# Kernel optimization log

Hardware: AMD Instinct MI355X
Metric: run time of the kernel (lower is better)

## Reference

```python
import jax, jax.numpy as jnp
import numpy as np

DIM = 768
NUM_HEADS = 16
HEAD_DIM = DIM // NUM_HEADS        # 48
AXIS_DIM = HEAD_DIM // 3           # 16 dims per spatial axis (t, y, x)
ROPE_BASE = 10000.0
T, H, W = 8, 14, 14                # N = 1568


def setup_inputs() -> dict:
    key = jax.random.key(0)
    k1, k2, k3 = jax.random.split(key, 3)
    B, N = 4, T * H * W
    x = jax.random.normal(k1, (B, N, DIM), dtype=jnp.float32)
    # 3D position grid (t, y, x) for each token
    t, y, xg = np.meshgrid(np.arange(T), np.arange(H), np.arange(W), indexing="ij")
    pos = jnp.asarray(np.stack([t.ravel(), y.ravel(), xg.ravel()], axis=-1), dtype=jnp.int32)  # [N,3]
    W_qkv = jax.random.normal(k2, (DIM, 3 * DIM), dtype=jnp.float32) * (DIM ** -0.5)
    W_proj = jax.random.normal(k3, (DIM, DIM), dtype=jnp.float32) * (DIM ** -0.5)
    b_proj = jnp.zeros((DIM,), dtype=jnp.float32)
    return {"x": x, "pos": pos, "W_qkv": W_qkv, "W_proj": W_proj, "b_proj": b_proj}


def _rope3d(q, k, pos):
    # q, k: [B, H, N, HEAD_DIM]; pos: [N, 3] int
    half = AXIS_DIM // 2  # 8 frequency pairs per axis
    inv_freq = ROPE_BASE ** (-jnp.arange(half, dtype=jnp.float32) / half)  # [half]
    # angles per axis: [N, 3, half]
    ang = pos.astype(jnp.float32)[:, :, None] * inv_freq[None, None, :]
    cos = jnp.cos(ang)  # [N, 3, half]
    sin = jnp.sin(ang)

    def rotate(t):
        # split head_dim into 3 axis chunks of AXIS_DIM, rotate_half within each
        t3 = t.reshape(*t.shape[:-1], 3, AXIS_DIM)          # [B,H,N,3,AXIS_DIM]
        t1, t2 = t3[..., :half], t3[..., half:]             # [B,H,N,3,half]
        c = cos[None, None]                                  # [1,1,N,3,half]
        s = sin[None, None]
        r = jnp.concatenate([t1 * c - t2 * s, t2 * c + t1 * s], axis=-1)
        return r.reshape(*t.shape)

    return rotate(q), rotate(k)


def reference(x, pos, W_qkv, W_proj, b_proj):
    B, N, C = x.shape
    scale = 1.0 / jnp.sqrt(jnp.asarray(HEAD_DIM, dtype=x.dtype))
    qkv = (x @ W_qkv).reshape(B, N, 3, NUM_HEADS, HEAD_DIM)
    qkv = jnp.transpose(qkv, (2, 0, 3, 1, 4))               # [3,B,H,N,Dh]
    q, k, v = qkv[0], qkv[1], qkv[2]
    q, k = _rope3d(q, k, pos)
    attn = jnp.einsum("bhnd,bhmd->bhnm", q, k) * scale      # [B,H,N,N]
    attn = jax.nn.softmax(attn, axis=-1)
    out = jnp.einsum("bhnm,bhmd->bhnd", attn, v)            # [B,H,N,Dh]
    out = jnp.transpose(out, (0, 2, 1, 3)).reshape(B, N, C)
    return out @ W_proj + b_proj
```

## Files before the change

kernel.cpp:

```cpp
#include <hip/hip_runtime.h>
#include <hip/hip_bf16.h>
#include <math.h>

#define DIM 768
#define NHEADS 16
#define HD 48
#define NTOK 1568
#define BATCH 4
#define ROWS (BATCH * NTOK)
#define QKV_COLS (3 * DIM)

typedef __attribute__((ext_vector_type(8))) _Float16 f16x8;
typedef __attribute__((ext_vector_type(2))) __fp16 fp16v2;
typedef __attribute__((ext_vector_type(4))) float f32x4;

__device__ inline ushort f2h(float f) {
    union { _Float16 h; ushort u; } v; v.h = (_Float16)f; return v.u;
}
__device__ inline float h2f(ushort u) {
    union { _Float16 h; ushort u; } v; v.u = u; return (float)v.h;
}

__device__ inline void gl16(const void* g, void* l) {
    __builtin_amdgcn_global_load_lds(
        (const __attribute__((address_space(1))) unsigned int*)g,
        (__attribute__((address_space(3))) unsigned int*)l, 16, 0, 0);
}

__global__ void cast_f32_f16(const float* __restrict__ in, ushort* __restrict__ out, int n4) {
    int i = blockIdx.x * blockDim.x + threadIdx.x;
    if (i >= n4) return;
    float4 v = ((const float4*)in)[i];
    ushort4 o;
    o.x = f2h(v.x); o.y = f2h(v.y); o.z = f2h(v.z); o.w = f2h(v.w);
    ((ushort4*)out)[i] = o;
}

__global__ void transpose_cast(const float* __restrict__ in, ushort* __restrict__ out,
                               int R, int C) {
    __shared__ ushort tile[32][33];
    int tx = threadIdx.x, ty = threadIdx.y;
    int c0 = blockIdx.x * 32, r0 = blockIdx.y * 32;
#pragma unroll
    for (int k = 0; k < 4; ++k)
        tile[ty + 8 * k][tx] = f2h(in[(size_t)(r0 + ty + 8 * k) * C + c0 + tx]);
    __syncthreads();
#pragma unroll
    for (int k = 0; k < 4; ++k)
        out[(size_t)(c0 + ty + 8 * k) * R + r0 + tx] = tile[tx][ty + 8 * k];
}

#define GBK 64

template <int BM>
__global__ __launch_bounds__(256) void gemm_f16(
    const ushort* __restrict__ A, const ushort* __restrict__ Bt,
    float* __restrict__ Cf, ushort* __restrict__ Cb, ushort* __restrict__ Vt,
    const float* __restrict__ bias, int M, int N, int K) {
    constexpr int MI = BM / 32;
    __shared__ ushort sA[2][BM * 64];
    __shared__ ushort sB[2][128 * 64];
    const int tid = threadIdx.x;
    const int wid = tid >> 6, lane = tid & 63;
    const int wm = wid >> 1, wn = wid & 1;
    const int m0 = blockIdx.y * BM, n0 = blockIdx.x * 128;
    const int lr = lane & 15, g = lane >> 4;

    auto STAGE = [&](int buf, int k0) {
#pragma unroll
        for (int i = 0; i < MI; ++i) {
            int c = tid + 256 * i;
            int row = c >> 3;
            int ch = (c & 7) ^ (row & 7);
            gl16(&A[(size_t)(m0 + row) * K + k0 + ch * 8], &sA[buf][(c & ~63) * 8]);
        }
#pragma unroll
        for (int i = 0; i < 4; ++i) {
            int c = tid + 256 * i;
            int row = c >> 3;
            int ch = (c & 7) ^ (row & 7);
            gl16(&Bt[(size_t)(n0 + row) * K + k0 + ch * 8], &sB[buf][(c & ~63) * 8]);
        }
    };

    f32x4 acc[MI][4] = {};
    const int NK = K / GBK;
    STAGE(0, 0);
    for (int t = 0; t < NK; ++t) {
        const int cur = t & 1;
        asm volatile("s_waitcnt vmcnt(0)" ::: "memory");
        __builtin_amdgcn_s_barrier();
        if (t + 1 < NK) STAGE(cur ^ 1, (t + 1) * GBK);
#pragma unroll
        for (int k2 = 0; k2 < GBK; k2 += 32) {
            f16x8 af[MI], bg[4];
#pragma unroll
            for (int f = 0; f < MI; ++f) {
                int ra = wm * (BM / 2) + f * 16 + lr;
                int ba = (ra * 128 + k2 * 2 + g * 16) ^ ((ra & 7) << 4);
                af[f] = *(const f16x8*)((const char*)sA[cur] + ba);
            }
#pragma unroll
            for (int f = 0; f < 4; ++f) {
                int rb = wn * 64 + f * 16 + lr;
                int bb = (rb * 128 + k2 * 2 + g * 16) ^ ((rb & 7) << 4);
                bg[f] = *(const f16x8*)((const char*)sB[cur] + bb);
            }
#pragma unroll
            for (int mi = 0; mi < MI; ++mi)
#pragma unroll
                for (int ni = 0; ni < 4; ++ni)
                    acc[mi][ni] = __builtin_amdgcn_mfma_f32_16x16x32_f16(
                        bg[ni], af[mi], acc[mi][ni], 0, 0, 0);
        }
    }
    const bool vpath = (Vt != nullptr) && (n0 >= 2 * DIM);
#pragma unroll
    for (int mi = 0; mi < MI; ++mi) {
        int m = m0 + wm * (BM / 2) + mi * 16 + lr;
#pragma unroll
        for (int ni = 0; ni < 4; ++ni) {
            int nb = n0 + wn * 64 + ni * 16 + g * 4;
            if (Cf) {
                float4 b4 = *(const float4*)&bias[nb];
                float4 o4;
                o4.x = acc[mi][ni][0] + b4.x;
                o4.y = acc[mi][ni][1] + b4.y;
                o4.z = acc[mi][ni][2] + b4.z;
                o4.w = acc[mi][ni][3] + b4.w;
                *(float4*)&Cf[(size_t)m * N + nb] = o4;
            } else if (vpath) {
                int bb = m / NTOK, tok = m % NTOK;
#pragma unroll
                for (int j = 0; j < 4; ++j)
                    Vt[((size_t)bb * DIM + (nb - 2 * DIM + j)) * NTOK + tok] =
                        f2h(acc[mi][ni][j]);
            } else {
                union { fp16v2 h; uint u; } c0, c1;
                c0.h = __builtin_amdgcn_cvt_pkrtz(acc[mi][ni][0], acc[mi][ni][1]);
                c1.h = __builtin_amdgcn_cvt_pkrtz(acc[mi][ni][2], acc[mi][ni][3]);
                uint2 uu; uu.x = c0.u; uu.y = c1.u;
                *(uint2*)&Cb[(size_t)m * N + nb] = uu;
            }
        }
    }
}

__global__ void rope_f16(ushort* __restrict__ qkv, const int* __restrict__ pos) {
    int idx = blockIdx.x * blockDim.x + threadIdx.x;
    const int total = BATCH * NTOK * NHEADS * 3;
    if (idx >= total) return;
    int axis = idx % 3; int t = idx / 3;
    int h = t & 15; t >>= 4;
    int n = t % NTOK; int b = t / NTOK;

    float p = (float)pos[n * 3 + axis];
    size_t base = ((size_t)b * NTOK + n) * QKV_COLS + h * HD + axis * 16;

    ushort lo[8], hi[8], klo[8], khi[8];
    *(ushort4*)&lo[0] = *(ushort4*)&qkv[base];
    *(ushort4*)&lo[4] = *(ushort4*)&qkv[base + 4];
    *(ushort4*)&hi[0] = *(ushort4*)&qkv[base + 8];
    *(ushort4*)&hi[4] = *(ushort4*)&qkv[base + 12];
    *(ushort4*)&klo[0] = *(ushort4*)&qkv[base + DIM];
    *(ushort4*)&klo[4] = *(ushort4*)&qkv[base + DIM + 4];
    *(ushort4*)&khi[0] = *(ushort4*)&qkv[base + DIM + 8];
    *(ushort4*)&khi[4] = *(ushort4*)&qkv[base + DIM + 12];

    const float RINV = 0.31622776601683794f;
    float fj = 1.0f;
#pragma unroll
    for (int j = 0; j < 8; ++j) {
        float s, c; __sincosf(p * fj, &s, &c); fj *= RINV;
        float q1 = h2f(lo[j]), q2 = h2f(hi[j]);
        lo[j] = f2h(q1 * c - q2 * s);
        hi[j] = f2h(q2 * c + q1 * s);
        float k1 = h2f(klo[j]), k2 = h2f(khi[j]);
        klo[j] = f2h(k1 * c - k2 * s);
        khi[j] = f2h(k2 * c + k1 * s);
    }
    *(ushort4*)&qkv[base] = *(ushort4*)&lo[0];
    *(ushort4*)&qkv[base + 4] = *(ushort4*)&lo[4];
    *(ushort4*)&qkv[base + 8] = *(ushort4*)&hi[0];
    *(ushort4*)&qkv[base + 12] = *(ushort4*)&hi[4];
    *(ushort4*)&qkv[base + DIM] = *(ushort4*)&klo[0];
    *(ushort4*)&qkv[base + DIM + 4] = *(ushort4*)&klo[4];
    *(ushort4*)&qkv[base + DIM + 8] = *(ushort4*)&khi[0];
    *(ushort4*)&qkv[base + DIM + 12] = *(ushort4*)&khi[4];
}

#define QBLK 128
#define KVB 32
#define NT (NTOK / KVB)
#define PP 40

__global__ __launch_bounds__(256) void attn_mfma(const ushort* __restrict__ qkv,
                                                 const ushort* __restrict__ vt,
                                                 ushort* __restrict__ aout) {
    __shared__ ushort sK3[3][KVB * 64];
    __shared__ ushort sV3[3][64 * 32];
    __shared__ ushort sP[4][32 * PP];
    const int tid = threadIdx.x, w = tid >> 6, lane = tid & 63;
    const int b = blockIdx.x >> 4, h = blockIdx.x & 15;
    const int q0 = blockIdx.y * QBLK;
    const size_t bbase = (size_t)b * NTOK * QKV_COLS;
    const size_t vbase = ((size_t)b * DIM + h * HD) * NTOK;
    const int lr = lane & 15, g = lane >> 4, lk = g << 3;
    const float qs = 0.14433756729740643f * 1.4426950408889634f;
    const float M2 = 14.0f;

    if (tid < 32) {
        sV3[0][48 * 32 + tid] = 0x3C00;
        sV3[1][48 * 32 + tid] = 0x3C00;
        sV3[2][48 * 32 + tid] = 0x3C00;
    }
    asm volatile("s_waitcnt lgkmcnt(0)" ::: "memory");

    f16x8 aq[2][2];
#pragma unroll
    for (int rb = 0; rb < 2; ++rb) {
        int qr = q0 + w * 32 + rb * 16 + lr;
        if (qr >= NTOK) qr = NTOK - 1;
        const ushort* qp = &qkv[bbase + (size_t)qr * QKV_COLS + h * HD];
        ushort r0[8], r1[8];
        *(ushort4*)&r0[0] = *(const ushort4*)&qp[lk];
        *(ushort4*)&r0[4] = *(const ushort4*)&qp[lk + 4];
        if (g < 2) {
            *(ushort4*)&r1[0] = *(const ushort4*)&qp[32 + lk];
            *(ushort4*)&r1[4] = *(const ushort4*)&qp[32 + lk + 4];
        } else {
#pragma unroll
            for (int e = 0; e < 8; ++e) r1[e] = 0;
        }
        f16x8 a0, a1;
#pragma unroll
        for (int e = 0; e < 8; ++e) {
            a0[e] = (_Float16)(h2f(r0[e]) * qs);
            a1[e] = (_Float16)(h2f(r1[e]) * qs);
        }
        aq[rb][0] = a0; aq[rb][1] = a1;
    }

    auto STAGE = [&](int buf, int kv0) {
        {
            int c = tid, row = c >> 3;
            int ch = (c & 7) ^ (row & 7);
            gl16(&qkv[bbase + (size_t)(kv0 + row) * QKV_COLS + DIM + h * HD + ch * 8],
                 &sK3[buf][(c & ~63) * 8]);
        }
        if (lane < 48) {
            int c = w * 48 + lane, d = c >> 2;
            int cc = (c & 3) ^ ((d >> 1) & 3);
            gl16(&vt[vbase + (size_t)d * NTOK + kv0 + cc * 8],
                 &sV3[buf][w * 384]);
        }
    };

    f32x4 o[2][4] = {};

    STAGE(0, 0);
    STAGE(1, KVB);
    for (int t = 0; t < NT; ++t) {
        const int cur = t % 3;
        if (t + 1 < NT) asm volatile("s_waitcnt vmcnt(2)" ::: "memory");
        else            asm volatile("s_waitcnt vmcnt(0)" ::: "memory");
        __builtin_amdgcn_s_barrier();
        if (t + 2 < NT) STAGE((t + 2) % 3, (t + 2) * KVB);

        f16x8 bk[2][2];
#pragma unroll
        for (int f = 0; f < 2; ++f)
#pragma unroll
            for (int ks = 0; ks < 2; ++ks) {
                int row = f * 16 + lr;
                int byt = (row * 128 + ks * 64 + g * 16) ^ ((lr & 7) << 4);
                bk[f][ks] = *(const f16x8*)((const char*)sK3[cur] + byt);
            }
        f32x4 sacc[2][2] = {{{-M2, -M2, -M2, -M2}, {-M2, -M2, -M2, -M2}},
                            {{-M2, -M2, -M2, -M2}, {-M2, -M2, -M2, -M2}}};
        __builtin_amdgcn_s_setprio(1);
#pragma unroll
        for (int rb = 0; rb < 2; ++rb)
#pragma unroll
            for (int f = 0; f < 2; ++f) {
                sacc[rb][f] = __builtin_amdgcn_mfma_f32_16x16x32_f16(bk[f][0], aq[rb][0], sacc[rb][f], 0, 0, 0);
                sacc[rb][f] = __builtin_amdgcn_mfma_f32_16x16x32_f16(bk[f][1], aq[rb][1], sacc[rb][f], 0, 0, 0);
            }
        __builtin_amdgcn_s_setprio(0);

#pragma unroll
        for (int rb = 0; rb < 2; ++rb)
#pragma unroll
            for (int f = 0; f < 2; ++f) {
                float p[4];
#pragma unroll
                for (int j = 0; j < 4; ++j) {
                    float pv;
                    asm("v_exp_f32 %0, %1" : "=v"(pv) : "v"(sacc[rb][f][j]));
                    p[j] = pv;
                }
                union { fp16v2 h; uint u; } c0, c1;
                c0.h = __builtin_amdgcn_cvt_pkrtz(p[0], p[1]);
                c1.h = __builtin_amdgcn_cvt_pkrtz(p[2], p[3]);
                uint2 uu; uu.x = c0.u; uu.y = c1.u;
                *(uint2*)&sP[w][(rb * 16 + lr) * PP + f * 16 + 4 * g] = uu;
            }

        f16x8 bv[4];
#pragma unroll
        for (int nf = 0; nf < 4; ++nf) {
            int row = nf * 16 + lr;
            int byt = (row * 64 + g * 16) ^ (((lr >> 1) & 3) << 4);
            bv[nf] = *(const f16x8*)((const char*)sV3[cur] + byt);
        }
        __builtin_amdgcn_s_setprio(1);
#pragma unroll
        for (int rb = 0; rb < 2; ++rb) {
            f16x8 pa = *(const f16x8*)&sP[w][(rb * 16 + lr) * PP + lk];
#pragma unroll
            for (int nf = 0; nf < 4; ++nf)
                o[rb][nf] = __builtin_amdgcn_mfma_f32_16x16x32_f16(bv[nf], pa, o[rb][nf], 0, 0, 0);
        }
        __builtin_amdgcn_s_setprio(0);
    }

#pragma unroll
    for (int rb = 0; rb < 2; ++rb) {
        float lv = __shfl(o[rb][3][0], lr, 64);
        int qr = q0 + w * 32 + rb * 16 + lr;
        if (qr < NTOK) {
            float inv = 1.f / lv;
            size_t rbse = ((size_t)b * NTOK + qr) * DIM;
#pragma unroll
            for (int nf = 0; nf < 3; ++nf) {
                ushort4 h4;
#pragma unroll
                for (int j = 0; j < 4; ++j)
                    ((ushort*)&h4)[j] = f2h(o[rb][nf][j] * inv);
                *(ushort4*)&aout[rbse + h * HD + nf * 16 + 4 * g] = h4;
            }
        }
    }
}

extern "C" void kernel_launch(void* const* d_in, const int* in_sizes, int n_in,
                              void* d_out, int out_size, void* d_ws, size_t ws_size,
                              hipStream_t stream) {
    const float* x   = (const float*)d_in[0];
    const int*   pos = (const int*)d_in[1];
    const float* Wq  = (const float*)d_in[2];
    const float* Wp  = (const float*)d_in[3];
    const float* bp  = (const float*)d_in[4];
    float* out = (float*)d_out;

    ushort* ws     = (ushort*)d_ws;
    ushort* x_h    = ws;
    ushort* WqT    = x_h + (size_t)ROWS * DIM;
    ushort* WpT    = WqT + (size_t)QKV_COLS * DIM;
    ushort* qkv_h  = WpT + (size_t)DIM * DIM;
    ushort* aout   = qkv_h + (size_t)ROWS * QKV_COLS;
    ushort* vt     = aout + (size_t)ROWS * DIM;

    cast_f32_f16<<<(ROWS * DIM / 4 + 255) / 256, 256, 0, stream>>>(x, x_h, ROWS * DIM / 4);
    transpose_cast<<<dim3(QKV_COLS / 32, DIM / 32), dim3(32, 8), 0, stream>>>(Wq, WqT, DIM, QKV_COLS);
    transpose_cast<<<dim3(DIM / 32, DIM / 32), dim3(32, 8), 0, stream>>>(Wp, WpT, DIM, DIM);

    gemm_f16<128><<<dim3(QKV_COLS / 128, ROWS / 128), 256, 0, stream>>>(
        x_h, WqT, nullptr, qkv_h, vt, nullptr, ROWS, QKV_COLS, DIM);

    rope_f16<<<(BATCH * NTOK * NHEADS * 3 + 255) / 256, 256, 0, stream>>>(qkv_h, pos);

    attn_mfma<<<dim3(BATCH * NHEADS, (NTOK + QBLK - 1) / QBLK), 256, 0, stream>>>(qkv_h, vt, aout);

    gemm_f16<64><<<dim3(DIM / 128, ROWS / 64), 256, 0, stream>>>(
        aout, WpT, out, nullptr, nullptr, bp, ROWS, DIM, DIM);
}
```

Baseline: 145.1 us.

## Fuse RoPE into QKV GEMM epilogue and software-pipeline attention softmax with QK

The separate rope_f16 kernel is removed. Rotary embedding is now applied inside the QKV GEMM epilogue, using a lane shuffle (xor 32) to fetch the paired half-dimension before the fp16 store. This drops a full read-modify-write pass over Q and K in global memory and one kernel launch. Separately, the attention loop is software-pipelined: each iteration issues the QK^T MFMAs for the current KV tile, then runs the exp/PV stage for the previous tile, so matrix ops can overlap with softmax. The price is more live registers (the previous scores and V fragments are carried across iterations) and extra sincos work in the GEMM epilogue.

```diff
diff --git a/kernel.cpp b/kernel.cpp
--- a/kernel.cpp
+++ b/kernel.cpp
@@ -56,7 +56,8 @@
 __global__ __launch_bounds__(256) void gemm_f16(
     const ushort* __restrict__ A, const ushort* __restrict__ Bt,
     float* __restrict__ Cf, ushort* __restrict__ Cb, ushort* __restrict__ Vt,
-    const float* __restrict__ bias, int M, int N, int K) {
+    const float* __restrict__ bias, const int* __restrict__ pos,
+    int M, int N, int K) {
     constexpr int MI = BM / 32;
     __shared__ ushort sA[2][BM * 64];
     __shared__ ushort sB[2][128 * 64];
@@ -115,6 +116,8 @@
         }
     }
     const bool vpath = (Vt != nullptr) && (n0 >= 2 * DIM);
+    const float RINV = 0.31622776601683794f;
+    const float RINV4 = 0.01f;
 #pragma unroll
     for (int mi = 0; mi < MI; ++mi) {
         int m = m0 + wm * (BM / 2) + mi * 16 + lr;
@@ -136,57 +139,30 @@
                     Vt[((size_t)bb * DIM + (nb - 2 * DIM + j)) * NTOK + tok] =
                         f2h(acc[mi][ni][j]);
             } else {
+                float vv[4];
+#pragma unroll
+                for (int j = 0; j < 4; ++j) vv[j] = acc[mi][ni][j];
+                if (pos) {
+                    int tok = m % NTOK;
+                    int axis = (nb >> 4) % 3;
+                    float p = (float)pos[tok * 3 + axis];
+                    float fj = (g & 1) ? RINV4 : 1.0f;
+                    bool hi = (g & 2) != 0;
+#pragma unroll
+                    for (int j = 0; j < 4; ++j) {
+                        float s, c; __sincosf(p * fj, &s, &c); fj *= RINV;
+                        float part = __shfl_xor(vv[j], 32);
+                        vv[j] = hi ? (vv[j] * c + part * s) : (vv[j] * c - part * s);
+                    }
+                }
                 union { fp16v2 h; uint u; } c0, c1;
-                c0.h = __builtin_amdgcn_cvt_pkrtz(acc[mi][ni][0], acc[mi][ni][1]);
-                c1.h = __builtin_amdgcn_cvt_pkrtz(acc[mi][ni][2], acc[mi][ni][3]);
+                c0.h = __builtin_amdgcn_cvt_pkrtz(vv[0], vv[1]);
+                c1.h = __builtin_amdgcn_cvt_pkrtz(vv[2], vv[3]);
                 uint2 uu; uu.x = c0.u; uu.y = c1.u;
                 *(uint2*)&Cb[(size_t)m * N + nb] = uu;
             }
         }
     }
-}
-
-__global__ void rope_f16(ushort* __restrict__ qkv, const int* __restrict__ pos) {
-    int idx = blockIdx.x * blockDim.x + threadIdx.x;
-    const int total = BATCH * NTOK * NHEADS * 3;
-    if (idx >= total) return;
-    int axis = idx % 3; int t = idx / 3;
-    int h = t & 15; t >>= 4;
-    int n = t % NTOK; int b = t / NTOK;
-
-    float p = (float)pos[n * 3 + axis];
-    size_t base = ((size_t)b * NTOK + n) * QKV_COLS + h * HD + axis * 16;
-
-    ushort lo[8], hi[8], klo[8], khi[8];
-    *(ushort4*)&lo[0] = *(ushort4*)&qkv[base];
-    *(ushort4*)&lo[4] = *(ushort4*)&qkv[base + 4];
-    *(ushort4*)&hi[0] = *(ushort4*)&qkv[base + 8];
-    *(ushort4*)&hi[4] = *(ushort4*)&qkv[base + 12];
-    *(ushort4*)&klo[0] = *(ushort4*)&qkv[base + DIM];
-    *(ushort4*)&klo[4] = *(ushort4*)&qkv[base + DIM + 4];
-    *(ushort4*)&khi[0] = *(ushort4*)&qkv[base + DIM + 8];
-    *(ushort4*)&khi[4] = *(ushort4*)&qkv[base + DIM + 12];
-
-    const float RINV = 0.31622776601683794f;
-    float fj = 1.0f;
-#pragma unroll
-    for (int j = 0; j < 8; ++j) {
-        float s, c; __sincosf(p * fj, &s, &c); fj *= RINV;
-        float q1 = h2f(lo[j]), q2 = h2f(hi[j]);
-        lo[j] = f2h(q1 * c - q2 * s);
-        hi[j] = f2h(q2 * c + q1 * s);
-        float k1 = h2f(klo[j]), k2 = h2f(khi[j]);
-        klo[j] = f2h(k1 * c - k2 * s);
-        khi[j] = f2h(k2 * c + k1 * s);
-    }
-    *(ushort4*)&qkv[base] = *(ushort4*)&lo[0];
-    *(ushort4*)&qkv[base + 4] = *(ushort4*)&lo[4];
-    *(ushort4*)&qkv[base + 8] = *(ushort4*)&hi[0];
-    *(ushort4*)&qkv[base + 12] = *(ushort4*)&hi[4];
-    *(ushort4*)&qkv[base + DIM] = *(ushort4*)&klo[0];
-    *(ushort4*)&qkv[base + DIM + 4] = *(ushort4*)&klo[4];
-    *(ushort4*)&qkv[base + DIM + 8] = *(ushort4*)&khi[0];
-    *(ushort4*)&qkv[base + DIM + 12] = *(ushort4*)&khi[4];
 }
 
 #define QBLK 128
@@ -256,38 +232,7 @@
         }
     };
 
-    f32x4 o[2][4] = {};
-
-    STAGE(0, 0);
-    STAGE(1, KVB);
-    for (int t = 0; t < NT; ++t) {
-        const int cur = t % 3;
-        if (t + 1 < NT) asm volatile("s_waitcnt vmcnt(2)" ::: "memory");
-        else            asm volatile("s_waitcnt vmcnt(0)" ::: "memory");
-        __builtin_amdgcn_s_barrier();
-        if (t + 2 < NT) STAGE((t + 2) % 3, (t + 2) * KVB);
-
-        f16x8 bk[2][2];
-#pragma unroll
-        for (int f = 0; f < 2; ++f)
-#pragma unroll
-            for (int ks = 0; ks < 2; ++ks) {
-                int row = f * 16 + lr;
-                int byt = (row * 128 + ks * 64 + g * 16) ^ ((lr & 7) << 4);
-                bk[f][ks] = *(const f16x8*)((const char*)sK3[cur] + byt);
-            }
-        f32x4 sacc[2][2] = {{{-M2, -M2, -M2, -M2}, {-M2, -M2, -M2, -M2}},
-                            {{-M2, -M2, -M2, -M2}, {-M2, -M2, -M2, -M2}}};
-        __builtin_amdgcn_s_setprio(1);
-#pragma unroll
-        for (int rb = 0; rb < 2; ++rb)
-#pragma unroll
-            for (int f = 0; f < 2; ++f) {
-                sacc[rb][f] = __builtin_amdgcn_mfma_f32_16x16x32_f16(bk[f][0], aq[rb][0], sacc[rb][f], 0, 0, 0);
-                sacc[rb][f] = __builtin_amdgcn_mfma_f32_16x16x32_f16(bk[f][1], aq[rb][1], sacc[rb][f], 0, 0, 0);
-            }
-        __builtin_amdgcn_s_setprio(0);
-
+    auto SOFTMAX_PV = [&](f32x4 sacc[2][2], f16x8 bvp[4], f32x4 o[2][4]) {
 #pragma unroll
         for (int rb = 0; rb < 2; ++rb)
 #pragma unroll
@@ -305,24 +250,70 @@
                 uint2 uu; uu.x = c0.u; uu.y = c1.u;
                 *(uint2*)&sP[w][(rb * 16 + lr) * PP + f * 16 + 4 * g] = uu;
             }
-
-        f16x8 bv[4];
+        asm volatile("s_waitcnt lgkmcnt(0)" ::: "memory");
+        __builtin_amdgcn_s_setprio(1);
+#pragma unroll
+        for (int rb = 0; rb < 2; ++rb) {
+            f16x8 pa = *(const f16x8*)&sP[w][(rb * 16 + lr) * PP + lk];
+#pragma unroll
+            for (int nf = 0; nf < 4; ++nf)
+                o[rb][nf] = __builtin_amdgcn_mfma_f32_16x16x32_f16(bvp[nf], pa, o[rb][nf], 0, 0, 0);
+        }
+        __builtin_amdgcn_s_setprio(0);
+    };
+
+    f32x4 o[2][4] = {};
+    f32x4 sacc_p[2][2];
+    f16x8 bvp[4];
+
+    STAGE(0, 0);
+    STAGE(1, KVB);
+    for (int t = 0; t < NT; ++t) {
+        const int cur = t % 3;
+        if (t + 1 < NT) asm volatile("s_waitcnt vmcnt(2)" ::: "memory");
+        else            asm volatile("s_waitcnt vmcnt(0)" ::: "memory");
+        __builtin_amdgcn_s_barrier();
+        if (t + 2 < NT) STAGE((t + 2) % 3, (t + 2) * KVB);
+
+        f16x8 bk[2][2];
+#pragma unroll
+        for (int f = 0; f < 2; ++f)
+#pragma unroll
+            for (int ks = 0; ks < 2; ++ks) {
+                int row = f * 16 + lr;
+                int byt = (row * 128 + ks * 64 + g * 16) ^ ((lr & 7) << 4);
+                bk[f][ks] = *(const f16x8*)((const char*)sK3[cur] + byt);
+            }
+        f16x8 bvc[4];
 #pragma unroll
         for (int nf = 0; nf < 4; ++nf) {
             int row = nf * 16 + lr;
             int byt = (row * 64 + g * 16) ^ (((lr >> 1) & 3) << 4);
-            bv[nf] = *(const f16x8*)((const char*)sV3[cur] + byt);
-        }
+            bvc[nf] = *(const f16x8*)((const char*)sV3[cur] + byt);
+        }
+
+        f32x4 sacc_c[2][2] = {{{-M2, -M2, -M2, -M2}, {-M2, -M2, -M2, -M2}},
+                              {{-M2, -M2, -M2, -M2}, {-M2, -M2, -M2, -M2}}};
         __builtin_amdgcn_s_setprio(1);
 #pragma unroll
-        for (int rb = 0; rb < 2; ++rb) {
-            f16x8 pa = *(const f16x8*)&sP[w][(rb * 16 + lr) * PP + lk];
-#pragma unroll
-            for (int nf = 0; nf < 4; ++nf)
-                o[rb][nf] = __builtin_amdgcn_mfma_f32_16x16x32_f16(bv[nf], pa, o[rb][nf], 0, 0, 0);
-        }
+        for (int rb = 0; rb < 2; ++rb)
+#pragma unroll
+            for (int f = 0; f < 2; ++f) {
+                sacc_c[rb][f] = __builtin_amdgcn_mfma_f32_16x16x32_f16(bk[f][0], aq[rb][0], sacc_c[rb][f], 0, 0, 0);
+                sacc_c[rb][f] = __builtin_amdgcn_mfma_f32_16x16x32_f16(bk[f][1], aq[rb][1], sacc_c[rb][f], 0, 0, 0);
+            }
         __builtin_amdgcn_s_setprio(0);
-    }
+
+        if (t > 0) SOFTMAX_PV(sacc_p, bvp, o);
+
+#pragma unroll
+        for (int rb = 0; rb < 2; ++rb)
+#pragma unroll
+            for (int f = 0; f < 2; ++f) sacc_p[rb][f] = sacc_c[rb][f];
+#pragma unroll
+        for (int nf = 0; nf < 4; ++nf) bvp[nf] = bvc[nf];
+    }
+    SOFTMAX_PV(sacc_p, bvp, o);
 
 #pragma unroll
     for (int rb = 0; rb < 2; ++rb) {
@@ -366,12 +357,10 @@
     transpose_cast<<<dim3(DIM / 32, DIM / 32), dim3(32, 8), 0, stream>>>(Wp, WpT, DIM, DIM);
 
     gemm_f16<128><<<dim3(QKV_COLS / 128, ROWS / 128), 256, 0, stream>>>(
-        x_h, WqT, nullptr, qkv_h, vt, nullptr, ROWS, QKV_COLS, DIM);
-
-    rope_f16<<<(BATCH * NTOK * NHEADS * 3 + 255) / 256, 256, 0, stream>>>(qkv_h, pos);
+        x_h, WqT, nullptr, qkv_h, vt, nullptr, pos, ROWS, QKV_COLS, DIM);
 
     attn_mfma<<<dim3(BATCH * NHEADS, (NTOK + QBLK - 1) / QBLK), 256, 0, stream>>>(qkv_h, vt, aout);
 
     gemm_f16<64><<<dim3(DIM / 128, ROWS / 64), 256, 0, stream>>>(
-        aout, WpT, out, nullptr, nullptr, bp, ROWS, DIM, DIM);
-}
+        aout, WpT, out, nullptr, nullptr, bp, nullptr, ROWS, DIM, DIM);
+}
```

Measured after the change: 168.6 us. 16.2% more time.
